# Performance work log

Hardware: AMD Instinct MI355X
Metric: run time of the kernel (lower is better)

## Reference

```python
import jax, jax.numpy as jnp
import numpy as np

B = 4096        # batch_size
D = 256         # feature_dim
N = 9000000     # dataset size (state buffer length)
G = 100         # num_groups
ALPHA = 0.5     # alpha_weight
GAMMA = 0.8
RHO = 8.0
LAM = 1.0       # lambada
ETA_P = 0.01
EPS = 1e-14
CLIP = 5.0


def setup_inputs() -> dict:
    key = jax.random.key(0)
    k = jax.random.split(key, 6)
    zis = jax.random.normal(k[0], (B, D), jnp.float32)
    zjs = jax.random.normal(k[1], (B, D), jnp.float32)
    # per-sample learned temperatures, small positive values
    taus_I = 0.01 + 0.2 * jax.random.uniform(k[2], (N,), jnp.float32)
    taus_T = 0.01 + 0.2 * jax.random.uniform(k[3], (N,), jnp.float32)
    group_info_I = jax.random.randint(k[4], (N,), 0, G, dtype=jnp.int32)
    group_info_T = jax.random.randint(k[5], (N,), 0, G, dtype=jnp.int32)
    ids = jnp.arange(B, dtype=jnp.int32)  # unique sample indices
    zeros_N = jnp.zeros((N,), jnp.float32)
    return {
        "zis": zis, "zjs": zjs,
        "s_I": zeros_N, "s_T": zeros_N, "b_I": zeros_N, "b_T": zeros_N,
        "z_I": jnp.zeros((G,), jnp.float32), "z_T": jnp.zeros((G,), jnp.float32),
        "p_I": jnp.ones((G,), jnp.float32) / G, "p_T": jnp.ones((G,), jnp.float32) / G,
        "taus_I": taus_I, "taus_T": taus_T,
        "ids": ids, "group_info_I": group_info_I, "group_info_T": group_info_T,
    }


def _l2norm(x):
    return x / jnp.maximum(jnp.linalg.norm(x, axis=1, keepdims=True), 1e-12)


def reference(zis, zjs, s_I, s_T, b_I, b_T, z_I, z_T, p_I, p_T,
              taus_I, taus_T, ids, group_info_I, group_info_T):
    zis = _l2norm(zis)
    zjs = _l2norm(zjs)
    sim = zis @ zjs.T                                   # [B, B]
    diag = jnp.diagonal(sim)                            # [B]
    mask_neg = 1.0 - jnp.eye(B, dtype=sim.dtype)
    image_diffs = sim - diag[:, None]
    text_diffs = sim - diag[None, :]

    tau_I = taus_I[ids]                                 # [B]
    tau_T = taus_T[ids]
    idt = jax.lax.stop_gradient(image_diffs / tau_I[:, None])
    tdt = jax.lax.stop_gradient(text_diffs / tau_T[None, :])

    # running max state (numerically-stable exp)
    old_b_I = b_I[ids]
    b_I_new = jnp.maximum(jnp.max(idt, axis=1), old_b_I)    # [B]
    old_b_T = b_T[ids]
    b_T_new = jnp.maximum(jnp.max(tdt, axis=0), old_b_T)    # [B]
    b_I = b_I.at[ids].set(b_I_new)
    b_T = b_T.at[ids].set(b_T_new)

    exp_I = jnp.exp(idt - b_I_new[:, None]) * mask_neg
    exp_T = jnp.exp(tdt - b_T_new[None, :]) * mask_neg
    g_I = jnp.sum(exp_I, axis=1)                         # [B]
    g_T = jnp.sum(exp_T, axis=0)                         # [B]

    # EMA of softmax denominators with max-rescaling
    s_I_new = (1.0 - GAMMA) * s_I[ids] * jnp.exp(old_b_I - b_I_new) + GAMMA * g_I
    s_T_new = (1.0 - GAMMA) * s_T[ids] * jnp.exp(old_b_T - b_T_new) + GAMMA * g_T
    s_I = s_I.at[ids].set(s_I_new)
    s_T = s_T.at[ids].set(s_T_new)
    s_I_c = jnp.maximum(s_I_new, EPS)
    s_T_c = jnp.maximum(s_T_new, EPS)

    w_I = exp_I / s_I_c[:, None]
    w_T = exp_T / s_T_c[None, :]

    gid_I = group_info_I[ids]                            # [B]
    gid_T = group_info_T[ids]
    gw_I = G * p_I[gid_I]                                # [B]
    gw_T = G * p_T[gid_T]

    image_loss = jnp.sum(w_I * gw_I[:, None] * image_diffs, axis=1)   # [B]
    text_loss = jnp.sum(w_T * gw_T[None, :] * text_diffs, axis=0)     # [B]
    total_loss = ALPHA * image_loss.mean() + (1.0 - ALPHA) * text_loss.mean()

    # per-group adversarial weight update
    F_I = tau_I * (jnp.log(s_I_c) + b_I_new + RHO)       # [B]
    F_T = tau_T * (jnp.log(s_T_c) + b_T_new + RHO)
    ones_b = jnp.ones((B,), sim.dtype)
    cnt_I = jnp.maximum(jax.ops.segment_sum(ones_b, gid_I, num_segments=G), 1.0)
    cnt_T = jnp.maximum(jax.ops.segment_sum(ones_b, gid_T, num_segments=G), 1.0)
    grad_p_I = jax.ops.segment_sum(F_I, gid_I, num_segments=G) / cnt_I
    grad_p_T = jax.ops.segment_sum(F_T, gid_T, num_segments=G) / cnt_T

    z_I = (1.0 - GAMMA) * z_I + GAMMA * grad_p_I
    z_T = (1.0 - GAMMA) * z_T + GAMMA * grad_p_T
    grad_hp_I = -LAM * jnp.log(p_I + EPS) - LAM
    grad_hp_T = -LAM * jnp.log(p_T + EPS) - LAM
    new_p_I = p_I * jnp.exp(2.0 * ETA_P * jnp.clip(z_I + grad_hp_I, -CLIP, CLIP))
    new_p_T = p_T * jnp.exp(2.0 * ETA_P * jnp.clip(z_T + grad_hp_T, -CLIP, CLIP))
    p_I = new_p_I / new_p_I.sum()
    p_T = new_p_T / new_p_T.sum()

    return total_loss, p_I, p_T
```

## Files before the change

kernel.cpp:

```cpp
#include <hip/hip_runtime.h>
#include <hip/hip_bf16.h>
#include <math.h>

#define BB 4096
#define DD 256
#define GG 100
#define GAMMA_C 0.8f
#define RHO_C 8.0f
#define ALPHA_C 0.5f
#define EPS_C 1e-14f
#define NSR 64
#define NSC 32

typedef __bf16 bf16x8 __attribute__((ext_vector_type(8)));
typedef float f32x16 __attribute__((ext_vector_type(16)));

__device__ inline int swzLoc(int r31, int k) {
    return ((k >> 4) << 9) | (((((k >> 3) & 1) << 5) | r31) << 3) | (k & 7);
}

__device__ inline float blockReduceSum(float v, float* lds) {
    for (int o = 32; o > 0; o >>= 1) v += __shfl_down(v, o);
    int lane = threadIdx.x & 63, wid = threadIdx.x >> 6;
    if (lane == 0) lds[wid] = v;
    __syncthreads();
    if (threadIdx.x == 0) {
        float r = lds[0];
        int nw = blockDim.x >> 6;
        for (int w = 1; w < nw; w++) r += lds[w];
        lds[0] = r;
    }
    __syncthreads();
    float r = lds[0];
    __syncthreads();
    return r;
}

__global__ void __launch_bounds__(256) norm_kernel(const float* __restrict__ zis,
                            const float* __restrict__ zjs,
                            ushort* __restrict__ zhi, ushort* __restrict__ zlo,
                            ushort* __restrict__ whi, ushort* __restrict__ wlo,
                            float* __restrict__ diag, float* __restrict__ acc) {
    __shared__ ushort st[4][4096];
    int rb = blockIdx.x;
    int wv = threadIdx.x >> 6, lane = threadIdx.x & 63;
    if (rb == 0) { acc[threadIdx.x] = 0.f; acc[threadIdx.x + 256] = 0.f; }
    for (int rr = 0; rr < 4; rr++) {
        int rloc = wv * 4 + rr;
        int r = rb * 16 + rloc;
        float4 zv = *(const float4*)&zis[r * DD + lane * 4];
        float4 wv4 = *(const float4*)&zjs[r * DD + lane * 4];
        float sz = zv.x * zv.x + zv.y * zv.y + zv.z * zv.z + zv.w * zv.w;
        float sw = wv4.x * wv4.x + wv4.y * wv4.y + wv4.z * wv4.z + wv4.w * wv4.w;
        float dt = zv.x * wv4.x + zv.y * wv4.y + zv.z * wv4.z + zv.w * wv4.w;
        for (int mask = 1; mask <= 32; mask <<= 1) {
            sz += __shfl_xor(sz, mask);
            sw += __shfl_xor(sw, mask);
            dt += __shfl_xor(dt, mask);
        }
        float iz = 1.0f / fmaxf(sqrtf(sz), 1e-12f);
        float iw = 1.0f / fmaxf(sqrtf(sw), 1e-12f);
        if (lane == 0) diag[r] = dt * iz * iw;
        float nz[4] = {zv.x * iz, zv.y * iz, zv.z * iz, zv.w * iz};
        float nw[4] = {wv4.x * iw, wv4.y * iw, wv4.z * iw, wv4.w * iw};
        for (int e = 0; e < 4; e++) {
            int k = lane * 4 + e;
            int li = ((k >> 4) << 8) | (((((k >> 3) & 1) << 4) | rloc) << 3) | (k & 7);
            __hip_bfloat16 hz = __float2bfloat16(nz[e]);
            __hip_bfloat16 lz = __float2bfloat16(nz[e] - __bfloat162float(hz));
            __hip_bfloat16 hw = __float2bfloat16(nw[e]);
            __hip_bfloat16 lw = __float2bfloat16(nw[e] - __bfloat162float(hw));
            st[0][li] = *(ushort*)&hz;
            st[1][li] = *(ushort*)&lz;
            st[2][li] = *(ushort*)&hw;
            st[3][li] = *(ushort*)&lw;
        }
    }
    __syncthreads();
    ushort* dsts[4] = {zhi, zlo, whi, wlo};
    int gbase = (rb >> 1) * 1024 + (rb & 1) * 16;
    for (int a = 0; a < 4; a++) {
        uint4* d = (uint4*)dsts[a];
        const uint4* s = (const uint4*)st[a];
        for (int it = 0; it < 2; it++) {
            int Lu = it * 256 + threadIdx.x;
            int Gu = gbase + (Lu >> 5) * 64 + ((Lu >> 4) & 1) * 32 + (Lu & 15);
            d[Gu] = s[Lu];
        }
    }
}

__global__ void __launch_bounds__(256, 4) fused_tile(const ushort* __restrict__ Ahi,
        const ushort* __restrict__ Alo, const ushort* __restrict__ Bhi,
        const ushort* __restrict__ Blo, const float* __restrict__ diag,
        const float* __restrict__ tausI, const float* __restrict__ tausT,
        const int* __restrict__ ids,
        float* __restrict__ pmR, float* __restrict__ pgR, float* __restrict__ pwR,
        float* __restrict__ pmC, float* __restrict__ pgC, float* __restrict__ pwC) {
    __shared__ float rDiag[128], rITau[128];
    __shared__ float cDiag[64], cITau[64];
    __shared__ float cmS[4][64], cgS[4][64], cwS[4][64];
    __shared__ float tr[4][32 * 65];

    int lane = threadIdx.x & 63;
    int wv = threadIdx.x >> 6;
    int bm = blockIdx.y * 128, bn = blockIdx.x * 64;
    int h = lane >> 5, cl = lane & 31;

    if (threadIdx.x < 128) {
        int r = bm + threadIdx.x;
        rDiag[threadIdx.x] = diag[r];
        rITau[threadIdx.x] = 1.0f / tausI[ids[r]];
    } else if (threadIdx.x < 192) {
        int c = bn + threadIdx.x - 128;
        cDiag[threadIdx.x - 128] = diag[c];
        cITau[threadIdx.x - 128] = 1.0f / tausT[ids[c]];
    }

    int aBase = (blockIdx.y * 4 + wv) * 8192;
    int b0 = (blockIdx.x * 2) * 8192;
    int b1 = b0 + 8192;
    int lofs = lane * 8;

    f32x16 acc[2] = {};
#pragma unroll
    for (int s = 0; s < 16; s++) {
        int so = s * 512 + lofs;
        bf16x8 ah  = *(const bf16x8*)&Ahi[aBase + so];
        bf16x8 al  = *(const bf16x8*)&Alo[aBase + so];
        bf16x8 bh0 = *(const bf16x8*)&Bhi[b0 + so];
        bf16x8 bl0 = *(const bf16x8*)&Blo[b0 + so];
        bf16x8 bh1 = *(const bf16x8*)&Bhi[b1 + so];
        bf16x8 bl1 = *(const bf16x8*)&Blo[b1 + so];
        acc[0] = __builtin_amdgcn_mfma_f32_32x32x16_bf16(ah, bh0, acc[0], 0, 0, 0);
        acc[1] = __builtin_amdgcn_mfma_f32_32x32x16_bf16(ah, bh1, acc[1], 0, 0, 0);
        acc[0] = __builtin_amdgcn_mfma_f32_32x32x16_bf16(ah, bl0, acc[0], 0, 0, 0);
        acc[1] = __builtin_amdgcn_mfma_f32_32x32x16_bf16(ah, bl1, acc[1], 0, 0, 0);
        acc[0] = __builtin_amdgcn_mfma_f32_32x32x16_bf16(al, bh0, acc[0], 0, 0, 0);
        acc[1] = __builtin_amdgcn_mfma_f32_32x32x16_bf16(al, bh1, acc[1], 0, 0, 0);
    }

    __syncthreads();
    float cd2[2], cit2[2], cbloc[2], cg[2] = {}, cw[2] = {};
#pragma unroll
    for (int u = 0; u < 2; u++) {
        int clc = u * 32 + cl;
        cd2[u] = cDiag[clc];
        cit2[u] = cITau[clc];
        float m = -INFINITY;
#pragma unroll
        for (int reg = 0; reg < 16; reg++) m = fmaxf(m, acc[u][reg]);
        m = fmaxf(m, __shfl_xor(m, 32));
        cbloc[u] = (m - cd2[u]) * cit2[u];
    }
#pragma unroll
    for (int u = 0; u < 2; u++) {
        int gc = bn + u * 32 + cl;
#pragma unroll
        for (int reg = 0; reg < 16; reg++) {
            int gr = bm + wv * 32 + (reg & 3) + 4 * h + 8 * (reg >> 2);
            float v = acc[u][reg];
            bool off = gr != gc;
            float dvT = v - cd2[u];
            float eT = off ? __expf(dvT * cit2[u] - cbloc[u]) : 0.f;
            cg[u] += eT;
            cw[u] += eT * dvT;
        }
    }
#pragma unroll
    for (int u = 0; u < 2; u++) {
        cg[u] += __shfl_xor(cg[u], 32);
        cw[u] += __shfl_xor(cw[u], 32);
        if (h == 0) {
            cmS[wv][u * 32 + cl] = cbloc[u];
            cgS[wv][u * 32 + cl] = cg[u];
            cwS[wv][u * 32 + cl] = cw[u];
        }
    }

#pragma unroll
    for (int u = 0; u < 2; u++)
#pragma unroll
        for (int reg = 0; reg < 16; reg++) {
            int r = (reg & 3) + 4 * h + 8 * (reg >> 2);
            tr[wv][r * 65 + u * 32 + cl] = acc[u][reg];
        }
    __syncthreads();

    if (threadIdx.x < 64) {
        int c = threadIdx.x;
        float m = fmaxf(fmaxf(cmS[0][c], cmS[1][c]), fmaxf(cmS[2][c], cmS[3][c]));
        float g = 0.f, w = 0.f;
        for (int wq = 0; wq < 4; wq++) {
            float f = __expf(cmS[wq][c] - m);
            g += cgS[wq][c] * f;
            w += cwS[wq][c] * f;
        }
        size_t o = (size_t)blockIdx.y * BB + bn + c;
        pmC[o] = m;
        pgC[o] = g;
        pwC[o] = w;
    }

    {
        int r = cl;
        int grow = bm + wv * 32 + r;
        float rd = rDiag[wv * 32 + r];
        float rit = rITau[wv * 32 + r];
        float vv[32];
#pragma unroll
        for (int j = 0; j < 32; j++) vv[j] = tr[wv][r * 65 + h * 32 + j];
        float m = -INFINITY;
#pragma unroll
        for (int j = 0; j < 32; j++) m = fmaxf(m, vv[j]);
        m = fmaxf(m, __shfl_xor(m, 32));
        float bloc = (m - rd) * rit;
        float rg = 0.f, rw = 0.f;
#pragma unroll
        for (int j = 0; j < 32; j++) {
            int gc = bn + h * 32 + j;
            float dv = vv[j] - rd;
            float e = (grow != gc) ? __expf(dv * rit - bloc) : 0.f;
            rg += e;
            rw += e * dv;
        }
        rg += __shfl_xor(rg, 32);
        rw += __shfl_xor(rw, 32);
        if (h == 0) {
            size_t o = (size_t)blockIdx.x * BB + grow;
            pmR[o] = bloc;
            pgR[o] = rg;
            pwR[o] = rw;
        }
    }
}

__global__ void __launch_bounds__(256) fin_kernel(
        const float* __restrict__ pmR, const float* __restrict__ pgR,
        const float* __restrict__ pwR, const float* __restrict__ pmC,
        const float* __restrict__ pgC, const float* __restrict__ pwC,
        const float* __restrict__ sI, const float* __restrict__ bI,
        const float* __restrict__ tausI, const int* __restrict__ gInfI,
        const float* __restrict__ pI,
        const float* __restrict__ sT, const float* __restrict__ bT,
        const float* __restrict__ tausT, const int* __restrict__ gInfT,
        const float* __restrict__ pT,
        const int* __restrict__ ids, float* __restrict__ acc,
        const float* __restrict__ zI, const float* __restrict__ zT,
        float* __restrict__ out) {
    __shared__ float lds[8];
    __shared__ float binF[GG], binC[GG];
    __shared__ float mS[8][32], gS[8][32], wS[8][32];
    __shared__ int lastFlag;
    if (threadIdx.x < GG) { binF[threadIdx.x] = 0.f; binC[threadIdx.x] = 0.f; }
    int side = blockIdx.x >> 7;
    int chunk = blockIdx.x & 127;
    int il = threadIdx.x & 31;
    int sg = threadIdx.x >> 5;
    int i = chunk * 32 + il;
    int ns = side ? NSC : NSR;
    const float* pm = side ? pmC : pmR;
    const float* pg = side ? pgC : pgR;
    const float* pw = side ? pwC : pwR;
    const float* sS = side ? sT : sI;
    const float* bS = side ? bT : bI;
    const float* taus = side ? tausT : tausI;
    const int* ginfo = side ? gInfT : gInfI;
    const float* pP = side ? pT : pI;

    float m = -INFINITY, g = 0.f, w = 0.f;
    for (int s = sg; s < ns; s += 8) {
        float pms = pm[(size_t)s * BB + i];
        float pgs = pg[(size_t)s * BB + i];
        float pws = pw[(size_t)s * BB + i];
        float mn = fmaxf(m, pms);
        float fo = __expf(m - mn);
        float fs = __expf(pms - mn);
        g = g * fo + pgs * fs;
        w = w * fo + pws * fs;
        m = mn;
    }
    mS[sg][il] = m;
    gS[sg][il] = g;
    wS[sg][il] = w;
    __syncthreads();

    float loss = 0.f;
    if (sg == 0) {
        int id = ids[i];
        float oldb = bS[id];
        float mm = mS[0][il];
        for (int q = 1; q < 8; q++) mm = fmaxf(mm, mS[q][il]);
        float bfin = fmaxf(mm, oldb);
        float gg2 = 0.f, ww2 = 0.f;
        for (int q = 0; q < 8; q++) {
            float f = __expf(mS[q][il] - bfin);
            gg2 += gS[q][il] * f;
            ww2 += wS[q][il] * f;
        }
        float tau = taus[id];
        float snew = (1.f - GAMMA_C) * sS[id] * expf(oldb - bfin) + GAMMA_C * gg2;
        float sc = fmaxf(snew, EPS_C);
        int gid = ginfo[id];
        float gw = (float)GG * pP[gid];
        loss = gw * ww2 / sc;
        float F = tau * (logf(sc) + bfin + RHO_C);
        atomicAdd(&binF[gid], F);
        atomicAdd(&binC[gid], 1.0f);
    }
    float lsum = blockReduceSum(loss, lds);
    if (threadIdx.x == 0) atomicAdd(&acc[side], lsum);
    __syncthreads();
    if (threadIdx.x < GG) {
        atomicAdd(&acc[2 + side * 200 + threadIdx.x], binF[threadIdx.x]);
        atomicAdd(&acc[102 + side * 200 + threadIdx.x], binC[threadIdx.x]);
    }

    __threadfence();
    if (threadIdx.x == 0) {
        int old = atomicAdd((int*)&acc[408], 1);
        lastFlag = (old == 255);
    }
    __syncthreads();
    if (!lastFlag) return;

    int gg = threadIdx.x;
    float npI = 0.f, npT = 0.f;
    if (gg < GG) {
        float cI = __hip_atomic_load(&acc[102 + gg], __ATOMIC_RELAXED, __HIP_MEMORY_SCOPE_AGENT);
        float fI = __hip_atomic_load(&acc[2 + gg], __ATOMIC_RELAXED, __HIP_MEMORY_SCOPE_AGENT);
        float gpI = fI / fmaxf(cI, 1.f);
        float zi = (1.f - GAMMA_C) * zI[gg] + GAMMA_C * gpI;
        float ghpI = -logf(pI[gg] + EPS_C) - 1.f;
        float ti = fminf(fmaxf(zi + ghpI, -5.f), 5.f);
        npI = pI[gg] * expf(0.02f * ti);

        float cT = __hip_atomic_load(&acc[302 + gg], __ATOMIC_RELAXED, __HIP_MEMORY_SCOPE_AGENT);
        float fT = __hip_atomic_load(&acc[202 + gg], __ATOMIC_RELAXED, __HIP_MEMORY_SCOPE_AGENT);
        float gpT = fT / fmaxf(cT, 1.f);
        float zt = (1.f - GAMMA_C) * zT[gg] + GAMMA_C * gpT;
        float ghpT = -logf(pT[gg] + EPS_C) - 1.f;
        float tt = fminf(fmaxf(zt + ghpT, -5.f), 5.f);
        npT = pT[gg] * expf(0.02f * tt);
    }
    float sumI = blockReduceSum(npI, lds);
    float sumT = blockReduceSum(npT, lds);
    if (gg < GG) {
        out[1 + gg] = npI / sumI;
        out[101 + gg] = npT / sumT;
    }
    if (gg == 0) {
        float lI = __hip_atomic_load(&acc[0], __ATOMIC_RELAXED, __HIP_MEMORY_SCOPE_AGENT);
        float lT = __hip_atomic_load(&acc[1], __ATOMIC_RELAXED, __HIP_MEMORY_SCOPE_AGENT);
        out[0] = ALPHA_C * (lI / (float)BB) + (1.f - ALPHA_C) * (lT / (float)BB);
    }
}

extern "C" void kernel_launch(void* const* d_in, const int* in_sizes, int n_in,
                              void* d_out, int out_size, void* d_ws, size_t ws_size,
                              hipStream_t stream) {
    const float* zis   = (const float*)d_in[0];
    const float* zjs   = (const float*)d_in[1];
    const float* s_I   = (const float*)d_in[2];
    const float* s_T   = (const float*)d_in[3];
    const float* b_I   = (const float*)d_in[4];
    const float* b_T   = (const float*)d_in[5];
    const float* z_I   = (const float*)d_in[6];
    const float* z_T   = (const float*)d_in[7];
    const float* p_I   = (const float*)d_in[8];
    const float* p_T   = (const float*)d_in[9];
    const float* tausI = (const float*)d_in[10];
    const float* tausT = (const float*)d_in[11];
    const int*   ids   = (const int*)d_in[12];
    const int*   gInfI = (const int*)d_in[13];
    const int*   gInfT = (const int*)d_in[14];
    float* out = (float*)d_out;

    char* ws = (char*)d_ws;
    ushort* zhi = (ushort*)ws;
    ushort* zlo = zhi + (size_t)BB * DD;
    ushort* whi = zlo + (size_t)BB * DD;
    ushort* wlo = whi + (size_t)BB * DD;
    float* acc  = (float*)(wlo + (size_t)BB * DD);
    float* diag = acc + 512;
    float* pmR  = diag + BB;
    float* pgR  = pmR + (size_t)NSR * BB;
    float* pwR  = pgR + (size_t)NSR * BB;
    float* pmC  = pwR + (size_t)NSR * BB;
    float* pgC  = pmC + (size_t)NSC * BB;
    float* pwC  = pgC + (size_t)NSC * BB;

    norm_kernel<<<256, 256, 0, stream>>>(zis, zjs, zhi, zlo, whi, wlo, diag, acc);
    fused_tile<<<dim3(64, 32), 256, 0, stream>>>(zhi, zlo, whi, wlo, diag,
            tausI, tausT, ids, pmR, pgR, pwR, pmC, pgC, pwC);
    fin_kernel<<<256, 256, 0, stream>>>(pmR, pgR, pwR, pmC, pgC, pwC,
            s_I, b_I, tausI, gInfI, p_I, s_T, b_T, tausT, gInfT, p_T, ids, acc,
            z_I, z_T, out);
}
```

Baseline: 272.8 us.

## Widen fused tile to 128x128 and merge row stats with online max rescaling

Each block now computes a 128x128 similarity tile instead of 128x64, so each A fragment is reused across four B fragments and the grid halves. The row-wise softmax statistics are built in two 64-column chunks through the LDS transpose buffer and merged with an online log-sum-exp rescale, including across the two half-wave lanes. This halves the number of row partials written and read by the finalize kernel. In exchange each wave holds twice the accumulators, which raises register pressure and can lower occupancy under the 4-blocks-per-SM launch bound.

```diff
diff --git a/kernel.cpp b/kernel.cpp
--- a/kernel.cpp
+++ b/kernel.cpp
@@ -9,15 +9,11 @@
 #define RHO_C 8.0f
 #define ALPHA_C 0.5f
 #define EPS_C 1e-14f
-#define NSR 64
+#define NSR 32
 #define NSC 32
 
 typedef __bf16 bf16x8 __attribute__((ext_vector_type(8)));
 typedef float f32x16 __attribute__((ext_vector_type(16)));
-
-__device__ inline int swzLoc(int r31, int k) {
-    return ((k >> 4) << 9) | (((((k >> 3) & 1) << 5) | r31) << 3) | (k & 7);
-}
 
 __device__ inline float blockReduceSum(float v, float* lds) {
     for (int o = 32; o > 0; o >>= 1) v += __shfl_down(v, o);
@@ -98,96 +94,86 @@
         float* __restrict__ pmR, float* __restrict__ pgR, float* __restrict__ pwR,
         float* __restrict__ pmC, float* __restrict__ pgC, float* __restrict__ pwC) {
     __shared__ float rDiag[128], rITau[128];
-    __shared__ float cDiag[64], cITau[64];
-    __shared__ float cmS[4][64], cgS[4][64], cwS[4][64];
+    __shared__ float cDiag[128], cITau[128];
+    __shared__ float cmS[4][128], cgS[4][128], cwS[4][128];
     __shared__ float tr[4][32 * 65];
 
     int lane = threadIdx.x & 63;
     int wv = threadIdx.x >> 6;
-    int bm = blockIdx.y * 128, bn = blockIdx.x * 64;
+    int bm = blockIdx.y * 128, bn = blockIdx.x * 128;
     int h = lane >> 5, cl = lane & 31;
 
     if (threadIdx.x < 128) {
         int r = bm + threadIdx.x;
         rDiag[threadIdx.x] = diag[r];
         rITau[threadIdx.x] = 1.0f / tausI[ids[r]];
-    } else if (threadIdx.x < 192) {
+    } else {
         int c = bn + threadIdx.x - 128;
         cDiag[threadIdx.x - 128] = diag[c];
         cITau[threadIdx.x - 128] = 1.0f / tausT[ids[c]];
     }
 
     int aBase = (blockIdx.y * 4 + wv) * 8192;
-    int b0 = (blockIdx.x * 2) * 8192;
-    int b1 = b0 + 8192;
+    int bB0 = (blockIdx.x * 4) * 8192;
     int lofs = lane * 8;
 
-    f32x16 acc[2] = {};
+    f32x16 acc[4] = {};
 #pragma unroll
     for (int s = 0; s < 16; s++) {
         int so = s * 512 + lofs;
-        bf16x8 ah  = *(const bf16x8*)&Ahi[aBase + so];
-        bf16x8 al  = *(const bf16x8*)&Alo[aBase + so];
-        bf16x8 bh0 = *(const bf16x8*)&Bhi[b0 + so];
-        bf16x8 bl0 = *(const bf16x8*)&Blo[b0 + so];
-        bf16x8 bh1 = *(const bf16x8*)&Bhi[b1 + so];
-        bf16x8 bl1 = *(const bf16x8*)&Blo[b1 + so];
-        acc[0] = __builtin_amdgcn_mfma_f32_32x32x16_bf16(ah, bh0, acc[0], 0, 0, 0);
-        acc[1] = __builtin_amdgcn_mfma_f32_32x32x16_bf16(ah, bh1, acc[1], 0, 0, 0);
-        acc[0] = __builtin_amdgcn_mfma_f32_32x32x16_bf16(ah, bl0, acc[0], 0, 0, 0);
-        acc[1] = __builtin_amdgcn_mfma_f32_32x32x16_bf16(ah, bl1, acc[1], 0, 0, 0);
-        acc[0] = __builtin_amdgcn_mfma_f32_32x32x16_bf16(al, bh0, acc[0], 0, 0, 0);
-        acc[1] = __builtin_amdgcn_mfma_f32_32x32x16_bf16(al, bh1, acc[1], 0, 0, 0);
-    }
-
-    __syncthreads();
-    float cd2[2], cit2[2], cbloc[2], cg[2] = {}, cw[2] = {};
-#pragma unroll
-    for (int u = 0; u < 2; u++) {
+        bf16x8 ah = *(const bf16x8*)&Ahi[aBase + so];
+        bf16x8 al = *(const bf16x8*)&Alo[aBase + so];
+        bf16x8 bh[4], bl[4];
+#pragma unroll
+        for (int j = 0; j < 4; j++) {
+            bh[j] = *(const bf16x8*)&Bhi[bB0 + j * 8192 + so];
+            bl[j] = *(const bf16x8*)&Blo[bB0 + j * 8192 + so];
+        }
+#pragma unroll
+        for (int j = 0; j < 4; j++)
+            acc[j] = __builtin_amdgcn_mfma_f32_32x32x16_bf16(ah, bh[j], acc[j], 0, 0, 0);
+#pragma unroll
+        for (int j = 0; j < 4; j++)
+            acc[j] = __builtin_amdgcn_mfma_f32_32x32x16_bf16(ah, bl[j], acc[j], 0, 0, 0);
+#pragma unroll
+        for (int j = 0; j < 4; j++)
+            acc[j] = __builtin_amdgcn_mfma_f32_32x32x16_bf16(al, bh[j], acc[j], 0, 0, 0);
+    }
+
+    __syncthreads();
+#pragma unroll
+    for (int u = 0; u < 4; u++) {
         int clc = u * 32 + cl;
-        cd2[u] = cDiag[clc];
-        cit2[u] = cITau[clc];
+        float cd = cDiag[clc];
+        float cit = cITau[clc];
         float m = -INFINITY;
 #pragma unroll
         for (int reg = 0; reg < 16; reg++) m = fmaxf(m, acc[u][reg]);
         m = fmaxf(m, __shfl_xor(m, 32));
-        cbloc[u] = (m - cd2[u]) * cit2[u];
-    }
-#pragma unroll
-    for (int u = 0; u < 2; u++) {
-        int gc = bn + u * 32 + cl;
+        float cb = (m - cd) * cit;
+        float cg = 0.f, cw = 0.f;
+        int gc = bn + clc;
 #pragma unroll
         for (int reg = 0; reg < 16; reg++) {
             int gr = bm + wv * 32 + (reg & 3) + 4 * h + 8 * (reg >> 2);
             float v = acc[u][reg];
             bool off = gr != gc;
-            float dvT = v - cd2[u];
-            float eT = off ? __expf(dvT * cit2[u] - cbloc[u]) : 0.f;
-            cg[u] += eT;
-            cw[u] += eT * dvT;
-        }
-    }
-#pragma unroll
-    for (int u = 0; u < 2; u++) {
-        cg[u] += __shfl_xor(cg[u], 32);
-        cw[u] += __shfl_xor(cw[u], 32);
+            float dvT = v - cd;
+            float eT = off ? __expf(dvT * cit - cb) : 0.f;
+            cg += eT;
+            cw += eT * dvT;
+        }
+        cg += __shfl_xor(cg, 32);
+        cw += __shfl_xor(cw, 32);
         if (h == 0) {
-            cmS[wv][u * 32 + cl] = cbloc[u];
-            cgS[wv][u * 32 + cl] = cg[u];
-            cwS[wv][u * 32 + cl] = cw[u];
-        }
-    }
-
-#pragma unroll
-    for (int u = 0; u < 2; u++)
-#pragma unroll
-        for (int reg = 0; reg < 16; reg++) {
-            int r = (reg & 3) + 4 * h + 8 * (reg >> 2);
-            tr[wv][r * 65 + u * 32 + cl] = acc[u][reg];
-        }
-    __syncthreads();
-
-    if (threadIdx.x < 64) {
+            cmS[wv][clc] = cb;
+            cgS[wv][clc] = cg;
+            cwS[wv][clc] = cw;
+        }
+    }
+    __syncthreads();
+
+    if (threadIdx.x < 128) {
         int c = threadIdx.x;
         float m = fmaxf(fmaxf(cmS[0][c], cmS[1][c]), fmaxf(cmS[2][c], cmS[3][c]));
         float g = 0.f, w = 0.f;
@@ -203,29 +189,49 @@
     }
 
     {
-        int r = cl;
-        int grow = bm + wv * 32 + r;
-        float rd = rDiag[wv * 32 + r];
-        float rit = rITau[wv * 32 + r];
-        float vv[32];
-#pragma unroll
-        for (int j = 0; j < 32; j++) vv[j] = tr[wv][r * 65 + h * 32 + j];
-        float m = -INFINITY;
-#pragma unroll
-        for (int j = 0; j < 32; j++) m = fmaxf(m, vv[j]);
-        m = fmaxf(m, __shfl_xor(m, 32));
-        float bloc = (m - rd) * rit;
-        float rg = 0.f, rw = 0.f;
-#pragma unroll
-        for (int j = 0; j < 32; j++) {
-            int gc = bn + h * 32 + j;
-            float dv = vv[j] - rd;
-            float e = (grow != gc) ? __expf(dv * rit - bloc) : 0.f;
-            rg += e;
-            rw += e * dv;
-        }
-        rg += __shfl_xor(rg, 32);
-        rw += __shfl_xor(rw, 32);
+        int grow = bm + wv * 32 + cl;
+        float rd = rDiag[wv * 32 + cl];
+        float rit = rITau[wv * 32 + cl];
+        float rm = -INFINITY, rg = 0.f, rw = 0.f;
+#pragma unroll
+        for (int ch = 0; ch < 2; ch++) {
+#pragma unroll
+            for (int uu = 0; uu < 2; uu++)
+#pragma unroll
+                for (int reg = 0; reg < 16; reg++) {
+                    int r = (reg & 3) + 4 * h + 8 * (reg >> 2);
+                    tr[wv][r * 65 + uu * 32 + cl] = acc[ch * 2 + uu][reg];
+                }
+            float vv[32];
+#pragma unroll
+            for (int j = 0; j < 32; j++) vv[j] = tr[wv][cl * 65 + h * 32 + j];
+            float m0 = -INFINITY;
+#pragma unroll
+            for (int j = 0; j < 32; j++) m0 = fmaxf(m0, vv[j]);
+            float g0 = 0.f, w0 = 0.f;
+#pragma unroll
+            for (int j = 0; j < 32; j++) {
+                int gc = bn + ch * 64 + h * 32 + j;
+                float dv = vv[j] - rd;
+                float e = (grow != gc) ? __expf((vv[j] - m0) * rit) : 0.f;
+                g0 += e;
+                w0 += e * dv;
+            }
+            float mn = fmaxf(rm, m0);
+            float fo = __expf((rm - mn) * rit);
+            float fs = __expf((m0 - mn) * rit);
+            rg = rg * fo + g0 * fs;
+            rw = rw * fo + w0 * fs;
+            rm = mn;
+        }
+        float mo = __shfl_xor(rm, 32);
+        float go = __shfl_xor(rg, 32);
+        float wo = __shfl_xor(rw, 32);
+        float mn = fmaxf(rm, mo);
+        rg = rg * __expf((rm - mn) * rit) + go * __expf((mo - mn) * rit);
+        rw = rw * __expf((rm - mn) * rit) + wo * __expf((mo - mn) * rit);
+        rm = mn;
+        float bloc = (rm - rd) * rit;
         if (h == 0) {
             size_t o = (size_t)blockIdx.x * BB + grow;
             pmR[o] = bloc;
@@ -391,7 +397,7 @@
     float* pwC  = pgC + (size_t)NSC * BB;
 
     norm_kernel<<<256, 256, 0, stream>>>(zis, zjs, zhi, zlo, whi, wlo, diag, acc);
-    fused_tile<<<dim3(64, 32), 256, 0, stream>>>(zhi, zlo, whi, wlo, diag,
+    fused_tile<<<dim3(32, 32), 256, 0, stream>>>(zhi, zlo, whi, wlo, diag,
             tausI, tausT, ids, pmR, pgR, pwR, pmC, pgC, pwC);
     fin_kernel<<<256, 256, 0, stream>>>(pmR, pgR, pwR, pmC, pgC, pwC,
             s_I, b_I, tausI, gInfI, p_I, s_T, b_T, tausT, gInfT, p_T, ids, acc,
```

Result: no change. 271.8 us (-0.4%).
